# Performance work log

Measured on AMD Instinct MI355X. Metric: run time of the kernel, lower is better.

## Reference

```python
import jax, jax.numpy as jnp
import numpy as np

BZ, P, T, H = 64, 512, 256, 768  # batch, bpe_seq_len, token seq_len, hidden


def setup_inputs() -> dict:
    key = jax.random.key(0)
    rng = np.random.default_rng(0)
    # variable number of tokens per sentence, each token -> 1 or 2 subwords
    tok_counts = rng.integers(200, T + 1, size=BZ)
    lens = rng.integers(1, 3, size=(BZ, T)).astype(np.int32)  # in {1,2}
    lens = np.where(np.arange(T)[None, :] < tok_counts[:, None], lens, 0)
    totals = lens.sum(axis=1)  # <= 512 == P by construction
    bert_mask = (np.arange(P)[None, :] < totals[:, None]).astype(np.int32)
    enc_out = jax.random.normal(key, (BZ, P, H), dtype=jnp.float32)
    return {
        "enc_out": enc_out,
        "bert_mask": jnp.asarray(bert_mask),
        "bert_lens": jnp.asarray(lens),
    }


def reference(enc_out, bert_mask, bert_lens):
    # enc_out: (BZ, P, H) last BERT hidden states (merge='none')
    # bert_mask: (BZ, P) int {0,1}; bert_lens: (BZ, T) subword counts per token
    bz, p_len, h = enc_out.shape
    t_len = bert_lens.shape[1]
    # cumulative subword counts; subword position p belongs to token
    # t = searchsorted(cum[b], p, 'right')  (zero-length tokens are skipped)
    cum = jnp.cumsum(bert_lens, axis=1)                      # (BZ, T)
    pos = jnp.arange(p_len)
    seg = jax.vmap(lambda c: jnp.searchsorted(c, pos, side='right'))(cum)  # (BZ, P)
    valid = bert_mask.astype(bool)
    dummy = bz * t_len  # trash segment for padding subword positions
    seg_global = jnp.where(valid, seg + jnp.arange(bz)[:, None] * t_len, dummy)
    sums = jax.ops.segment_sum(
        enc_out.reshape(-1, h), seg_global.reshape(-1), num_segments=bz * t_len + 1
    )[: bz * t_len]                                          # (BZ*T, H)
    counts = jnp.maximum(bert_lens.reshape(-1, 1), 1).astype(enc_out.dtype)
    out = (sums / counts).reshape(bz, t_len, h)
    # masked_scatter semantics: positions with lens==0 stay zero
    return jnp.where((bert_lens > 0)[..., None], out, jnp.zeros((), enc_out.dtype))
```

## Files before the change

### kernel.cpp

```cpp
#include <hip/hip_runtime.h>

#define BZ 64
#define P  512
#define T  256
#define H  768
#define H4 (H / 4)

__global__ void scan_kernel(const int* __restrict__ lens, int* __restrict__ starts) {
    __shared__ int sm[T];
    const int b = blockIdx.x;
    const int t = threadIdx.x;
    const int v = lens[b * T + t];
    sm[t] = v;
    __syncthreads();
    #pragma unroll
    for (int off = 1; off < T; off <<= 1) {
        const int add = (t >= off) ? sm[t - off] : 0;
        __syncthreads();
        sm[t] += add;
        __syncthreads();
    }
    starts[b * T + t] = sm[t] - v;
}

__global__ void gather_kernel(const float* __restrict__ enc,
                              const int* __restrict__ lens,
                              const int* __restrict__ starts,
                              float* __restrict__ out) {
    const int idx = blockIdx.x * blockDim.x + threadIdx.x;
    const int h4  = idx % H4;
    const int bt  = idx / H4;
    const int b   = bt / T;

    const int len = lens[bt];
    float4 r = make_float4(0.f, 0.f, 0.f, 0.f);
    if (len > 0) {
        const int start = starts[bt];
        const float4* row =
            (const float4*)(enc + ((size_t)b * P + (size_t)start) * H) + h4;
        r = row[0];
        if (len > 1) {
            #pragma unroll 1
            for (int k = 1; k < len; ++k) {
                const float4 r2 = row[(size_t)k * H4];
                r.x += r2.x; r.y += r2.y; r.z += r2.z; r.w += r2.w;
            }
            const float inv = 1.0f / (float)len;
            r.x *= inv; r.y *= inv; r.z *= inv; r.w *= inv;
        }
    }
    ((float4*)out)[idx] = r;
}

extern "C" void kernel_launch(void* const* d_in, const int* in_sizes, int n_in,
                              void* d_out, int out_size, void* d_ws, size_t ws_size,
                              hipStream_t stream) {
    const float* enc   = (const float*)d_in[0];
    const int*   lens  = (const int*)d_in[2];
    float*       out   = (float*)d_out;
    int*         start = (int*)d_ws;

    scan_kernel<<<BZ, T, 0, stream>>>(lens, start);

    const int total4 = BZ * T * H4;
    gather_kernel<<<total4 / 256, 256, 0, stream>>>(enc, lens, start, out);
}
```

Before: 156.3 us.

## Fuse prefix-scan and gather into one kernel with per-block redundant scan

Merges the separate scan kernel and gather kernel into a single launch. Each block recomputes the batch row's prefix sum of subword lengths in shared memory, then handles a chunk of 16 tokens, reading lens and starts from LDS instead of global memory. This drops one kernel launch and the workspace round-trip. In exchange it adds a redundant 256-wide scan in every block, and the grid shrinks to 1024 blocks that each loop 12 times, which reduces parallelism.

```diff
diff --git a/kernel.cpp b/kernel.cpp
--- a/kernel.cpp
+++ b/kernel.cpp
@@ -5,63 +5,72 @@
 #define T  256
 #define H  768
 #define H4 (H / 4)
+#define CHUNKS 16
+#define TOK_PER_CHUNK (T / CHUNKS)
+#define F4_PER_CHUNK (TOK_PER_CHUNK * H4)
+#define ITERS (F4_PER_CHUNK / 256)
 
-__global__ void scan_kernel(const int* __restrict__ lens, int* __restrict__ starts) {
-    __shared__ int sm[T];
-    const int b = blockIdx.x;
-    const int t = threadIdx.x;
-    const int v = lens[b * T + t];
-    sm[t] = v;
+__global__ __launch_bounds__(256)
+void fused_bert_merge(const float* __restrict__ enc,
+                      const int* __restrict__ lens,
+                      float* __restrict__ out) {
+    __shared__ int s_incl[T];
+    __shared__ int s_len[T];
+
+    const int b     = blockIdx.x >> 4;
+    const int chunk = blockIdx.x & (CHUNKS - 1);
+    const int tid   = threadIdx.x;
+
+    const int v = lens[b * T + tid];
+    s_len[tid]  = v;
+    s_incl[tid] = v;
     __syncthreads();
     #pragma unroll
     for (int off = 1; off < T; off <<= 1) {
-        const int add = (t >= off) ? sm[t - off] : 0;
+        const int add = (tid >= off) ? s_incl[tid - off] : 0;
         __syncthreads();
-        sm[t] += add;
+        s_incl[tid] += add;
         __syncthreads();
     }
-    starts[b * T + t] = sm[t] - v;
-}
 
-__global__ void gather_kernel(const float* __restrict__ enc,
-                              const int* __restrict__ lens,
-                              const int* __restrict__ starts,
-                              float* __restrict__ out) {
-    const int idx = blockIdx.x * blockDim.x + threadIdx.x;
-    const int h4  = idx % H4;
-    const int bt  = idx / H4;
-    const int b   = bt / T;
+    const int t0 = chunk * TOK_PER_CHUNK;
+    const float4* encb = (const float4*)(enc + (size_t)b * P * H);
+    float4* outb       = (float4*)(out + ((size_t)b * T + t0) * H);
 
-    const int len = lens[bt];
-    float4 r = make_float4(0.f, 0.f, 0.f, 0.f);
-    if (len > 0) {
-        const int start = starts[bt];
-        const float4* row =
-            (const float4*)(enc + ((size_t)b * P + (size_t)start) * H) + h4;
-        r = row[0];
-        if (len > 1) {
-            #pragma unroll 1
-            for (int k = 1; k < len; ++k) {
-                const float4 r2 = row[(size_t)k * H4];
-                r.x += r2.x; r.y += r2.y; r.z += r2.z; r.w += r2.w;
+    #pragma unroll
+    for (int it = 0; it < ITERS; ++it) {
+        const int i    = it * 256 + tid;
+        const int trel = i / H4;
+        const int h4   = i - trel * H4;
+        const int tok  = t0 + trel;
+
+        const int len   = s_len[tok];
+        const int start = s_incl[tok] - len;
+
+        float4 r = make_float4(0.f, 0.f, 0.f, 0.f);
+        if (len > 0) {
+            const float4* row = encb + (size_t)start * H4 + h4;
+            r = row[0];
+            if (len > 1) {
+                #pragma unroll 1
+                for (int k = 1; k < len; ++k) {
+                    const float4 r2 = row[(size_t)k * H4];
+                    r.x += r2.x; r.y += r2.y; r.z += r2.z; r.w += r2.w;
+                }
+                const float inv = 1.0f / (float)len;
+                r.x *= inv; r.y *= inv; r.z *= inv; r.w *= inv;
             }
-            const float inv = 1.0f / (float)len;
-            r.x *= inv; r.y *= inv; r.z *= inv; r.w *= inv;
         }
+        outb[i] = r;
     }
-    ((float4*)out)[idx] = r;
 }
 
 extern "C" void kernel_launch(void* const* d_in, const int* in_sizes, int n_in,
                               void* d_out, int out_size, void* d_ws, size_t ws_size,
                               hipStream_t stream) {
-    const float* enc   = (const float*)d_in[0];
-    const int*   lens  = (const int*)d_in[2];
-    float*       out   = (float*)d_out;
-    int*         start = (int*)d_ws;
+    const float* enc  = (const float*)d_in[0];
+    const int*   lens = (const int*)d_in[2];
+    float*       out  = (float*)d_out;
 
-    scan_kernel<<<BZ, T, 0, stream>>>(lens, start);
-
-    const int total4 = BZ * T * H4;
-    gather_kernel<<<total4 / 256, 256, 0, stream>>>(enc, lens, start, out);
+    fused_bert_merge<<<BZ * CHUNKS, 256, 0, stream>>>(enc, lens, out);
 }
```

Measured after the change: 158.3 us. Within noise of the previous version (+1.3%).
